# Kernel optimization log

Measured on AMD Instinct MI355X. Metric: run time of the kernel, lower is better.

## Reference

```python
import jax, jax.numpy as jnp
import numpy as np

KH, KW, STRIDE, PAD = 3, 3, 1, 1


def unfold(img, kh, kw, stride, padding):
    # torch.nn.functional.unfold, transposed to [B, L, C*kh*kw] with (c, kh, kw)-major ordering
    b, c, h, w = img.shape
    p = jnp.pad(img, ((0, 0), (0, 0), (padding, padding), (padding, padding)))
    oh = (h - kh + 2 * padding) // stride + 1
    ow = (w - kw + 2 * padding) // stride + 1
    # [b, c, kh*kw, oh, ow]; static python loop over the 9 kernel offsets only
    cols = jnp.stack([p[:, :, i:i + oh * stride:stride, j:j + ow * stride:stride]
                      for i in range(kh) for j in range(kw)], axis=2)
    return cols.reshape(b, c * kh * kw, oh * ow).transpose(0, 2, 1), oh, ow


def setup_inputs() -> dict:
    key = jax.random.key(0)
    k1, k2 = jax.random.split(key)
    img = jax.random.normal(k1, (8, 64, 112, 112), dtype=jnp.float32)
    weights = 0.8 * jax.random.normal(k2, (64, 64, 3, 3), dtype=jnp.float32)
    return {"img": img, "weights": weights}


def reference(img, weights):
    b = img.shape[0]
    O = weights.shape[0]
    W = weights.reshape(O, -1)            # [O, K], K = in_ch*kh*kw
    K = W.shape[1]
    u, oh, ow = unfold(img, KH, KW, STRIDE, PAD)   # [b, L, K]
    u2 = u * u
    u3 = u2 * u

    def gemm(poly):
        return jnp.einsum('blk,ok->blo', poly, W)

    # f: identity-kernel term has all-zero coefficients (p00=p10=p20=p30=0) -> drops out
    f = gemm(-0.000287 + 0.266 * u - 0.1097 * u2) / 75

    # identity_kernel is all ones, so (const*ones) @ ones.T == const * K (scalar)
    g1 = (0.11 / 75) * K + gemm(0.001309 + 0.00619 * u - 0.009 * u2 + 0.001383 * u3)
    g2 = (0.179 / 75) * K + gemm(-0.0025 + 0.00303 * u - 0.00484 * u2 + 0.0175 * u3)
    g3 = (0.238 / 75) * K + gemm(-0.000954 + 0.00187 * u + 0.001877 * u2 + 0.01502 * u3)
    g4 = (0.388 / 75) * K + gemm(-0.00734 + 0.001117 * u + 0.00752 * u2 + 0.009 * u3)
    g5 = (0.507 / 75) * K + gemm(-0.01017 + 0.000426 * u + 0.00837 * u2 + 0.00413 * u3)

    sig = jax.nn.sigmoid
    s1 = sig(10 * (0.15 - f))
    s2 = sig(10 * (f - 0.15)) + sig(10 * (0.23 - f)) - 1
    s3 = sig(10 * (f - 0.23)) + sig(10 * (0.32 - f)) - 1
    s4 = sig(10 * (f - 0.32)) + sig(10 * (0.39 - f)) - 1
    s5 = sig(10 * (f - 0.39))

    out = s1 * g1 + s2 * g2 + s3 * g3 + s4 * g4 + s5 * g5   # [b, L, O]
    return out.transpose(0, 2, 1).reshape(b, O, oh, ow)
```

## Files before the change

### kernel.cpp

```cpp
#include <hip/hip_runtime.h>

#define HW   112
#define PH   114
#define KK   576
#define ROWB (PH * 128)
#define PLANE_SH (8 * PH * PH * 64)
#define PLANE_B  (PLANE_SH * 2)
#define WB_OFF_SH (3 * PLANE_SH)
#define S_OFF_SH  (WB_OFF_SH + 36864)

typedef __attribute__((ext_vector_type(8))) short s16x8;
typedef __attribute__((ext_vector_type(4))) float f32x4;
typedef __attribute__((ext_vector_type(2))) float f32x2;
typedef __attribute__((address_space(3))) unsigned int lds_u32;
typedef const __attribute__((address_space(1))) unsigned int glb_u32;

__device__ inline unsigned short f2bf(float f) {
    unsigned u = __float_as_uint(f);
    u += 0x7FFF + ((u >> 16) & 1);
    return (unsigned short)(u >> 16);
}

__global__ void prep_all(const float* __restrict__ W,
                         unsigned short* __restrict__ pw,
                         unsigned short* __restrict__ wb,
                         float* __restrict__ S) {
    __shared__ float partial[256];
    const int bid = blockIdx.x, t = threadIdx.x;
    if (bid < 24) {
        const int p = bid >> 3, b = bid & 7;
        unsigned short* base = pw + (size_t)p * PLANE_SH + (size_t)b * PH * PH * 64;
        const s16x8 z = {0, 0, 0, 0, 0, 0, 0, 0};
        for (int i = 0; i < 15; ++i) {
            const int e = t + i * 256;
            if (e >= 3616) break;
            const int n = e >> 3, c8 = e & 7;
            int x, yy;
            if (n < 114)      { yy = 0;   x = n; }
            else if (n < 228) { yy = 113; x = n - 114; }
            else { const int m2 = n - 228; yy = 1 + (m2 >> 1); x = (m2 & 1) ? 113 : 0; }
            *(s16x8*)&base[(yy * PH + x) * 64 + c8 * 8] = z;
        }
    } else if (bid < 168) {
        const int i   = (bid - 24) * 256 + t;
        const int j   = i & 7;
        const int l   = (i >> 3) & 63;
        const int nt  = (i >> 9) & 3;
        const int cc  = (i >> 11) & 1;
        const int tap = i >> 12;
        const int c   = cc * 32 + ((l >> 4) << 3) + j;
        const int o   = nt * 16 + (l & 15);
        wb[i] = f2bf(W[o * KK + c * 9 + tap]);
    } else {
        const int o = t >> 2, part = t & 3;
        const float4* row = (const float4*)(W + o * KK) + part * 36;
        float s = 0.f;
        for (int k = 0; k < 36; ++k) { float4 v = row[k]; s += v.x + v.y + v.z + v.w; }
        partial[t] = s;
        __syncthreads();
        if (part == 0) S[o] = partial[t] + partial[t + 1] + partial[t + 2] + partial[t + 3];
    }
}

__global__ __launch_bounds__(256) void pow_kernel(const float* __restrict__ img,
                                                  unsigned short* __restrict__ pw) {
    __shared__ __align__(16) unsigned short sA[3 * 112 * 72];
    const int t = threadIdx.x;
    const int bid = blockIdx.x;
    const int b = bid / 112, y = bid - b * 112;

    const int c = t & 63, xq0 = t >> 6;
    const float4* src = (const float4*)(img + (((size_t)(b * 64 + c) * HW + y) * HW));
    #pragma unroll
    for (int i = 0; i < 7; ++i) {
        const int xq = xq0 + i * 4;
        const float4 v = src[xq];
        const float vv[4] = {v.x, v.y, v.z, v.w};
        #pragma unroll
        for (int u = 0; u < 4; ++u) {
            const float v1 = vv[u], v2 = v1 * v1, v3 = v2 * v1;
            const int x = xq * 4 + u;
            sA[x * 72 + c]         = f2bf(v1);
            sA[8064 + x * 72 + c]  = f2bf(v2);
            sA[16128 + x * 72 + c] = f2bf(v3);
        }
    }
    __syncthreads();

    for (int i = 0; i < 11; ++i) {
        const int ch = t + i * 256;
        if (ch >= 2688) break;
        const int p = ch / 896, r = ch - p * 896;
        const int x = r >> 3, c8 = r & 7;
        const s16x8 val = *(const s16x8*)&sA[p * 8064 + x * 72 + c8 * 8];
        *(s16x8*)&pw[(size_t)p * PLANE_SH + ((size_t)(b * PH + y + 1) * PH + (x + 1)) * 64 + c8 * 8] = val;
    }
}

#define LP_PLANE 11520
#define LP_ROW   1152
#define STAGE_B  34560

__global__ __launch_bounds__(256, 2) void conv_main(const unsigned short* __restrict__ pw,
                                                    const unsigned short* __restrict__ wb,
                                                    const float* __restrict__ S,
                                                    float* __restrict__ out) {
    __shared__ __align__(16) char tile[STAGE_B];

    const int t = threadIdx.x, wv = t >> 6, lane = t & 63;
    const int m = lane & 15, q = lane >> 4;

    const int bid = blockIdx.x;
    const int b = bid & 7;
    const int r = bid >> 3;
    const int ty = r / 7, tx = r - ty * 7;
    const int y0 = ty * 8, x0 = tx * 16;

    f32x4 acc[3][2][4];
    #pragma unroll
    for (int p = 0; p < 3; ++p)
        #pragma unroll
        for (int at = 0; at < 2; ++at)
            #pragma unroll
            for (int nt = 0; nt < 4; ++nt)
                acc[p][at][nt] = (f32x4){0.f, 0.f, 0.f, 0.f};

    const char* pwin = (const char*)pw + ((size_t)(b * PH + y0) * PH + x0) * 128;

    #pragma unroll 1
    for (int cc = 0; cc < 2; ++cc) {
        if (cc) __syncthreads();
        #pragma unroll
        for (int i = 0; i < 9; ++i) {
            const int f = i * 4096 + t * 16;
            if (f < STAGE_B) {
                const int p   = f / LP_PLANE;
                const int r1  = f - p * LP_PLANE;
                const int row = r1 / LP_ROW;
                const int r2  = r1 - row * LP_ROW;
                const int px  = r2 >> 6;
                const int c8s = (r2 >> 4) & 3;
                const int c8  = c8s ^ (px & 3) ^ ((px >> 2) & 3);
                const char* gp = pwin + (size_t)p * PLANE_B + row * ROWB + px * 128 + cc * 64 + c8 * 16;
                lds_u32* lp = (lds_u32*)(tile + i * 4096 + wv * 1024);
                __builtin_amdgcn_global_load_lds((glb_u32*)gp, lp, 16, 0, 0);
            }
        }
        __syncthreads();

        #pragma unroll
        for (int kx = 0; kx < 3; ++kx) {
            s16x8 bf[3][4];
            #pragma unroll
            for (int ky = 0; ky < 3; ++ky) {
                const int tap = ky * 3 + kx;
                #pragma unroll
                for (int nt = 0; nt < 4; ++nt)
                    bf[ky][nt] = *(const s16x8*)&wb[(((tap * 2 + cc) * 4 + nt) * 64 + lane) * 8];
            }
            const int pxr  = m + kx;
            const int c8sr = q ^ (pxr & 3) ^ ((pxr >> 2) & 3);
            const int abase = wv * (2 * LP_ROW) + pxr * 64 + c8sr * 16;
            s16x8 af[4][3];
            #pragma unroll
            for (int r4 = 0; r4 < 4; ++r4)
                #pragma unroll
                for (int p = 0; p < 3; ++p)
                    af[r4][p] = *(const s16x8*)&tile[abase + r4 * LP_ROW + p * LP_PLANE];
            #pragma unroll
            for (int ky = 0; ky < 3; ++ky)
                #pragma unroll
                for (int at = 0; at < 2; ++at)
                    #pragma unroll
                    for (int p = 0; p < 3; ++p)
                        #pragma unroll
                        for (int nt = 0; nt < 4; ++nt)
                            acc[p][at][nt] = __builtin_amdgcn_mfma_f32_16x16x32_bf16(
                                af[at + ky][p], bf[ky][nt], acc[p][at][nt], 0, 0, 0);
        }
    }

    #pragma unroll
    for (int nt = 0; nt < 4; ++nt) {
        const int o = nt * 16 + (lane & 15);
        const float Sv = S[o];
        const float fS = -0.000287f / 75.f * Sv;
        const float cg1 = 0.8448f  + 0.001309f * Sv;
        const float D1  = 0.52992f - 0.003809f * Sv;
        const float D2  = 0.45312f + 0.001546f * Sv;
        const float D3  = 1.152f   - 0.006386f * Sv;
        const float D4  = 0.91392f - 0.00283f  * Sv;
        #pragma unroll
        for (int at = 0; at < 2; ++at) {
            float res[4];
            #pragma unroll
            for (int h = 0; h < 2; ++h) {
                const f32x2 u1 = {acc[0][at][nt][2 * h], acc[0][at][nt][2 * h + 1]};
                const f32x2 u2 = {acc[1][at][nt][2 * h], acc[1][at][nt][2 * h + 1]};
                const f32x2 u3 = {acc[2][at][nt][2 * h], acc[2][at][nt][2 * h + 1]};
                const f32x2 f  = fS   + 0.00354667f * u1 - 0.00146267f * u2;
                const f32x2 g1 = cg1  + 0.00619f    * u1 - 0.009f      * u2 + 0.001383f * u3;
                const f32x2 d1 = D1   - 0.00316f    * u1 + 0.00416f    * u2 + 0.016117f * u3;
                const f32x2 d2 = D2   - 0.00116f    * u1 + 0.006717f   * u2 - 0.00248f  * u3;
                const f32x2 d3 = D3   - 0.000753f   * u1 + 0.005643f   * u2 - 0.00602f  * u3;
                const f32x2 d4 = D4   - 0.000691f   * u1 + 0.00085f    * u2 - 0.00487f  * u3;
                f32x2 E;
                E.x = __expf(-10.f * f.x);
                E.y = __expf(-10.f * f.y);
                const f32x2 den1 = 1.f + E * 4.4816890703f;
                const f32x2 den2 = 1.f + E * 9.9741824548f;
                const f32x2 den3 = 1.f + E * 24.5325301971f;
                const f32x2 den4 = 1.f + E * 49.4024491055f;
                f32x2 o2 = g1;
                o2.x += __builtin_amdgcn_rcpf(den1.x) * d1.x + __builtin_amdgcn_rcpf(den2.x) * d2.x
                      + __builtin_amdgcn_rcpf(den3.x) * d3.x + __builtin_amdgcn_rcpf(den4.x) * d4.x;
                o2.y += __builtin_amdgcn_rcpf(den1.y) * d1.y + __builtin_amdgcn_rcpf(den2.y) * d2.y
                      + __builtin_amdgcn_rcpf(den3.y) * d3.y + __builtin_amdgcn_rcpf(den4.y) * d4.y;
                res[2 * h] = o2.x; res[2 * h + 1] = o2.y;
            }
            const int y = y0 + 2 * wv + at;
            float* op = out + (((size_t)(b * 64 + o)) * HW + y) * HW + x0 + q * 4;
            *(float4*)op = make_float4(res[0], res[1], res[2], res[3]);
        }
    }
}

extern "C" void kernel_launch(void* const* d_in, const int* in_sizes, int n_in,
                              void* d_out, int out_size, void* d_ws, size_t ws_size,
                              hipStream_t stream) {
    const float* img = (const float*)d_in[0];
    const float* w   = (const float*)d_in[1];
    float* outp = (float*)d_out;
    unsigned short* pw = (unsigned short*)d_ws;
    unsigned short* wb = pw + WB_OFF_SH;
    float* S = (float*)(pw + S_OFF_SH);

    hipLaunchKernelGGL(prep_all,   dim3(169), dim3(256), 0, stream, w, pw, wb, S);
    hipLaunchKernelGGL(pow_kernel, dim3(896), dim3(256), 0, stream, img, pw);
    hipLaunchKernelGGL(conv_main,  dim3(784), dim3(256), 0, stream, pw, wb, S, outp);
}
```

Measured before the change: 120.9 us.

## Split output channels across blocks, stage weights in LDS, merge prep kernels

```diff
diff --git a/kernel.cpp b/kernel.cpp
--- a/kernel.cpp
+++ b/kernel.cpp
@@ -21,14 +21,43 @@
     return (unsigned short)(u >> 16);
 }
 
-__global__ void prep_all(const float* __restrict__ W,
-                         unsigned short* __restrict__ pw,
-                         unsigned short* __restrict__ wb,
-                         float* __restrict__ S) {
-    __shared__ float partial[256];
+__global__ __launch_bounds__(256) void prep_pow(const float* __restrict__ img,
+                                                const float* __restrict__ W,
+                                                unsigned short* __restrict__ pw,
+                                                unsigned short* __restrict__ wb,
+                                                float* __restrict__ S) {
+    __shared__ __align__(16) unsigned short sA[3 * 112 * 72];
     const int bid = blockIdx.x, t = threadIdx.x;
-    if (bid < 24) {
-        const int p = bid >> 3, b = bid & 7;
+    if (bid < 896) {
+        const int b = bid / 112, y = bid - b * 112;
+        const int c = t & 63, xq0 = t >> 6;
+        const float4* src = (const float4*)(img + (((size_t)(b * 64 + c) * HW + y) * HW));
+        #pragma unroll
+        for (int i = 0; i < 7; ++i) {
+            const int xq = xq0 + i * 4;
+            const float4 v = src[xq];
+            const float vv[4] = {v.x, v.y, v.z, v.w};
+            #pragma unroll
+            for (int u = 0; u < 4; ++u) {
+                const float v1 = vv[u], v2 = v1 * v1, v3 = v2 * v1;
+                const int x = xq * 4 + u;
+                sA[x * 72 + c]         = f2bf(v1);
+                sA[8064 + x * 72 + c]  = f2bf(v2);
+                sA[16128 + x * 72 + c] = f2bf(v3);
+            }
+        }
+        __syncthreads();
+        for (int i = 0; i < 11; ++i) {
+            const int ch = t + i * 256;
+            if (ch >= 2688) break;
+            const int p = ch / 896, r = ch - p * 896;
+            const int x = r >> 3, c8 = r & 7;
+            const s16x8 val = *(const s16x8*)&sA[p * 8064 + x * 72 + c8 * 8];
+            *(s16x8*)&pw[(size_t)p * PLANE_SH + ((size_t)(b * PH + y + 1) * PH + (x + 1)) * 64 + c8 * 8] = val;
+        }
+    } else if (bid < 920) {
+        const int k = bid - 896;
+        const int p = k >> 3, b = k & 7;
         unsigned short* base = pw + (size_t)p * PLANE_SH + (size_t)b * PH * PH * 64;
         const s16x8 z = {0, 0, 0, 0, 0, 0, 0, 0};
         for (int i = 0; i < 15; ++i) {
@@ -41,8 +70,8 @@
             else { const int m2 = n - 228; yy = 1 + (m2 >> 1); x = (m2 & 1) ? 113 : 0; }
             *(s16x8*)&base[(yy * PH + x) * 64 + c8 * 8] = z;
         }
-    } else if (bid < 168) {
-        const int i   = (bid - 24) * 256 + t;
+    } else if (bid < 1064) {
+        const int i   = (bid - 920) * 256 + t;
         const int j   = i & 7;
         const int l   = (i >> 3) & 63;
         const int nt  = (i >> 9) & 3;
@@ -52,6 +81,7 @@
         const int o   = nt * 16 + (l & 15);
         wb[i] = f2bf(W[o * KK + c * 9 + tap]);
     } else {
+        __shared__ float partial[256];
         const int o = t >> 2, part = t & 3;
         const float4* row = (const float4*)(W + o * KK) + part * 36;
         float s = 0.f;
@@ -62,49 +92,16 @@
     }
 }
 
-__global__ __launch_bounds__(256) void pow_kernel(const float* __restrict__ img,
-                                                  unsigned short* __restrict__ pw) {
-    __shared__ __align__(16) unsigned short sA[3 * 112 * 72];
-    const int t = threadIdx.x;
-    const int bid = blockIdx.x;
-    const int b = bid / 112, y = bid - b * 112;
-
-    const int c = t & 63, xq0 = t >> 6;
-    const float4* src = (const float4*)(img + (((size_t)(b * 64 + c) * HW + y) * HW));
-    #pragma unroll
-    for (int i = 0; i < 7; ++i) {
-        const int xq = xq0 + i * 4;
-        const float4 v = src[xq];
-        const float vv[4] = {v.x, v.y, v.z, v.w};
-        #pragma unroll
-        for (int u = 0; u < 4; ++u) {
-            const float v1 = vv[u], v2 = v1 * v1, v3 = v2 * v1;
-            const int x = xq * 4 + u;
-            sA[x * 72 + c]         = f2bf(v1);
-            sA[8064 + x * 72 + c]  = f2bf(v2);
-            sA[16128 + x * 72 + c] = f2bf(v3);
-        }
-    }
-    __syncthreads();
-
-    for (int i = 0; i < 11; ++i) {
-        const int ch = t + i * 256;
-        if (ch >= 2688) break;
-        const int p = ch / 896, r = ch - p * 896;
-        const int x = r >> 3, c8 = r & 7;
-        const s16x8 val = *(const s16x8*)&sA[p * 8064 + x * 72 + c8 * 8];
-        *(s16x8*)&pw[(size_t)p * PLANE_SH + ((size_t)(b * PH + y + 1) * PH + (x + 1)) * 64 + c8 * 8] = val;
-    }
-}
-
 #define LP_PLANE 11520
 #define LP_ROW   1152
 #define STAGE_B  34560
-
-__global__ __launch_bounds__(256, 2) void conv_main(const unsigned short* __restrict__ pw,
+#define WH_B     18432
+
+__global__ __launch_bounds__(256, 3) void conv_main(const unsigned short* __restrict__ pw,
                                                     const unsigned short* __restrict__ wb,
                                                     const float* __restrict__ S,
                                                     float* __restrict__ out) {
+    __shared__ __align__(16) char ldsw[WH_B];
     __shared__ __align__(16) char tile[STAGE_B];
 
     const int t = threadIdx.x, wv = t >> 6, lane = t & 63;
@@ -112,24 +109,38 @@
 
     const int bid = blockIdx.x;
     const int b = bid & 7;
-    const int r = bid >> 3;
+    const int rest = bid >> 3;
+    const int oc2 = rest & 1;
+    const int r = rest >> 1;
     const int ty = r / 7, tx = r - ty * 7;
     const int y0 = ty * 8, x0 = tx * 16;
 
-    f32x4 acc[3][2][4];
+    f32x4 acc[3][2][2];
     #pragma unroll
     for (int p = 0; p < 3; ++p)
         #pragma unroll
         for (int at = 0; at < 2; ++at)
             #pragma unroll
-            for (int nt = 0; nt < 4; ++nt)
-                acc[p][at][nt] = (f32x4){0.f, 0.f, 0.f, 0.f};
+            for (int ntl = 0; ntl < 2; ++ntl)
+                acc[p][at][ntl] = (f32x4){0.f, 0.f, 0.f, 0.f};
 
     const char* pwin = (const char*)pw + ((size_t)(b * PH + y0) * PH + x0) * 128;
 
     #pragma unroll 1
     for (int cc = 0; cc < 2; ++cc) {
         if (cc) __syncthreads();
+        #pragma unroll
+        for (int i = 0; i < 5; ++i) {
+            const int f = i * 4096 + t * 16;
+            if (f < WH_B) {
+                const int lchunk = f >> 10;
+                const int tap = lchunk >> 1, ntl = lchunk & 1;
+                const char* gp = (const char*)wb
+                    + ((size_t)((tap * 2 + cc) * 4 + oc2 * 2 + ntl)) * 1024 + lane * 16;
+                lds_u32* lp = (lds_u32*)(ldsw + i * 4096 + wv * 1024);
+                __builtin_amdgcn_global_load_lds((glb_u32*)gp, lp, 16, 0, 0);
+            }
+        }
         #pragma unroll
         for (int i = 0; i < 9; ++i) {
             const int f = i * 4096 + t * 16;
@@ -150,14 +161,12 @@
 
         #pragma unroll
         for (int kx = 0; kx < 3; ++kx) {
-            s16x8 bf[3][4];
-            #pragma unroll
-            for (int ky = 0; ky < 3; ++ky) {
-                const int tap = ky * 3 + kx;
+            s16x8 bf[3][2];
+            #pragma unroll
+            for (int ky = 0; ky < 3; ++ky)
                 #pragma unroll
-                for (int nt = 0; nt < 4; ++nt)
-                    bf[ky][nt] = *(const s16x8*)&wb[(((tap * 2 + cc) * 4 + nt) * 64 + lane) * 8];
-            }
+                for (int ntl = 0; ntl < 2; ++ntl)
+                    bf[ky][ntl] = *(const s16x8*)&ldsw[(((ky * 3 + kx) * 2 + ntl) << 10) + lane * 16];
             const int pxr  = m + kx;
             const int c8sr = q ^ (pxr & 3) ^ ((pxr >> 2) & 3);
             const int abase = wv * (2 * LP_ROW) + pxr * 64 + c8sr * 16;
@@ -174,15 +183,15 @@
                     #pragma unroll
                     for (int p = 0; p < 3; ++p)
                         #pragma unroll
-                        for (int nt = 0; nt < 4; ++nt)
-                            acc[p][at][nt] = __builtin_amdgcn_mfma_f32_16x16x32_bf16(
-                                af[at + ky][p], bf[ky][nt], acc[p][at][nt], 0, 0, 0);
+                        for (int ntl = 0; ntl < 2; ++ntl)
+                            acc[p][at][ntl] = __builtin_amdgcn_mfma_f32_16x16x32_bf16(
+                                af[at + ky][p], bf[ky][ntl], acc[p][at][ntl], 0, 0, 0);
         }
     }
 
     #pragma unroll
-    for (int nt = 0; nt < 4; ++nt) {
-        const int o = nt * 16 + (lane & 15);
+    for (int ntl = 0; ntl < 2; ++ntl) {
+        const int o = (oc2 * 2 + ntl) * 16 + (lane & 15);
         const float Sv = S[o];
         const float fS = -0.000287f / 75.f * Sv;
         const float cg1 = 0.8448f  + 0.001309f * Sv;
@@ -195,9 +204,9 @@
             float res[4];
             #pragma unroll
             for (int h = 0; h < 2; ++h) {
-                const f32x2 u1 = {acc[0][at][nt][2 * h], acc[0][at][nt][2 * h + 1]};
-                const f32x2 u2 = {acc[1][at][nt][2 * h], acc[1][at][nt][2 * h + 1]};
-                const f32x2 u3 = {acc[2][at][nt][2 * h], acc[2][at][nt][2 * h + 1]};
+                const f32x2 u1 = {acc[0][at][ntl][2 * h], acc[0][at][ntl][2 * h + 1]};
+                const f32x2 u2 = {acc[1][at][ntl][2 * h], acc[1][at][ntl][2 * h + 1]};
+                const f32x2 u3 = {acc[2][at][ntl][2 * h], acc[2][at][ntl][2 * h + 1]};
                 const f32x2 f  = fS   + 0.00354667f * u1 - 0.00146267f * u2;
                 const f32x2 g1 = cg1  + 0.00619f    * u1 - 0.009f      * u2 + 0.001383f * u3;
                 const f32x2 d1 = D1   - 0.00316f    * u1 + 0.00416f    * u2 + 0.016117f * u3;
@@ -235,7 +244,6 @@
     unsigned short* wb = pw + WB_OFF_SH;
     float* S = (float*)(pw + S_OFF_SH);
 
-    hipLaunchKernelGGL(prep_all,   dim3(169), dim3(256), 0, stream, w, pw, wb, S);
-    hipLaunchKernelGGL(pow_kernel, dim3(896), dim3(256), 0, stream, img, pw);
-    hipLaunchKernelGGL(conv_main,  dim3(784), dim3(256), 0, stream, pw, wb, S, outp);
-}
+    hipLaunchKernelGGL(prep_pow,  dim3(1065), dim3(256), 0, stream, img, w, pw, wb, S);
+    hipLaunchKernelGGL(conv_main, dim3(1568), dim3(256), 0, stream, pw, wb, S, outp);
+}
```

New measurement: 114.4 us. 5.4% less time.
